# Kernel optimization log

Hardware: AMD Instinct MI355X
Metric: run time of the kernel (lower is better)

The kernel has to match this reference:

```python
import jax, jax.numpy as jnp
import numpy as np

B, S, D, H = 2, 2048, 2048, 16
DK = D // H
THETA = 10000.0


def setup_inputs() -> dict:
    key = jax.random.key(0)
    ks = jax.random.split(key, 5)
    scale = 0.02
    return {
        "x": jax.random.normal(ks[0], (B, S, D), dtype=jnp.float32),
        "W_Q": jax.random.normal(ks[1], (D, D), dtype=jnp.float32) * scale,
        "W_K": jax.random.normal(ks[2], (D, D), dtype=jnp.float32) * scale,
        "W_V": jax.random.normal(ks[3], (D, D), dtype=jnp.float32) * scale,
        "W_O": jax.random.normal(ks[4], (D, D), dtype=jnp.float32) * scale,
        "token_positions": jnp.arange(S, dtype=jnp.int32),
    }


def _rope(x, pos):
    # x: [B, S, H, DK]; pos: [S]. Interleaved-pair rotation (cs336 RoPE).
    half = DK // 2
    inv_freq = THETA ** (-(jnp.arange(half, dtype=jnp.float32) / half))  # [half]
    ang = pos.astype(jnp.float32)[:, None] * inv_freq[None, :]           # [S, half]
    cos = jnp.cos(ang)[None, :, None, :]                                 # [1,S,1,half]
    sin = jnp.sin(ang)[None, :, None, :]
    x1, x2 = x[..., ::2], x[..., 1::2]
    r1 = x1 * cos - x2 * sin
    r2 = x1 * sin + x2 * cos
    return jnp.stack([r1, r2], axis=-1).reshape(x.shape)


def reference(x, W_Q, W_K, W_V, W_O, token_positions):
    # QKV projections (Linear with no bias: y = x @ W^T)
    Q = (x @ W_Q.T).reshape(B, S, H, DK)
    K = (x @ W_K.T).reshape(B, S, H, DK)
    V = (x @ W_V.T).reshape(B, S, H, DK)
    Q = _rope(Q, token_positions)
    K = _rope(K, token_positions)
    scores = jnp.einsum("bqhd,bkhd->bhqk", Q, K) / jnp.sqrt(jnp.float32(DK))
    causal = jnp.tril(jnp.ones((S, S), dtype=bool))  # True = attend
    scores = jnp.where(causal[None, None], scores, -jnp.inf)
    attn = jax.nn.softmax(scores, axis=-1)
    out = jnp.einsum("bhqk,bkhd->bqhd", attn, V).reshape(B, S, D)
    return out @ W_O.T
```

## Files before the change

### kernel.cpp

```cpp
#include <hip/hip_runtime.h>
#include <hip/hip_bf16.h>
#include <cstdint>
#include <cstddef>

#define B_ 2
#define S_ 2048
#define D_ 2048
#define H_ 16
#define DK_ 128
#define M_ (B_*S_)

typedef __attribute__((ext_vector_type(8))) __bf16 bf16x8;
typedef __attribute__((ext_vector_type(4))) float f32x4;
typedef __attribute__((ext_vector_type(16))) float f32x16;

__device__ __forceinline__ unsigned short f2bf(float f) {
  union { float f; unsigned int u; } v; v.f = f;
  unsigned int r = (v.u + 0x7fffu + ((v.u >> 16) & 1u)) >> 16;
  return (unsigned short)r;
}
__device__ __forceinline__ float bf2f(unsigned short b) {
  union { unsigned int u; float f; } v; v.u = ((unsigned int)b) << 16;
  return v.f;
}

__device__ __forceinline__ void gld16(const void* g, void* l) {
  __builtin_amdgcn_global_load_lds(
      (const __attribute__((address_space(1))) unsigned int*)g,
      (__attribute__((address_space(3))) unsigned int*)l, 16, 0, 0);
}

__global__ void cvt_bf16(const float* __restrict__ src, unsigned short* __restrict__ dst, int n) {
  int i = (blockIdx.x * blockDim.x + threadIdx.x) * 4;
  if (i + 3 < n) {
    float4 v = *(const float4*)(src + i);
    dst[i+0] = f2bf(v.x); dst[i+1] = f2bf(v.y);
    dst[i+2] = f2bf(v.z); dst[i+3] = f2bf(v.w);
  }
}

template<int WRITE_BF16>
__global__ __launch_bounds__(512, 2) void gemm8p(const unsigned short* __restrict__ A,
                                                 const unsigned short* __restrict__ W0,
                                                 const unsigned short* __restrict__ W1,
                                                 const unsigned short* __restrict__ W2,
                                                 void* __restrict__ C0, void* __restrict__ C1,
                                                 void* __restrict__ C2,
                                                 int M, int N, int K) {
  __shared__ unsigned short sA[2][2][256 * 32];
  __shared__ unsigned short sB[2][2][256 * 32];
  const int z = blockIdx.z;
  const unsigned short* Bt = (z == 0) ? W0 : (z == 1) ? W1 : W2;
  void* Cout = (z == 0) ? C0 : (z == 1) ? C1 : C2;

  const int tid  = threadIdx.x;
  const int lane = tid & 63;
  const int wid  = tid >> 6;
  const int wm = wid >> 2, wn = wid & 3;
  const int l16 = lane & 15, quad = lane >> 4;
  const int col16 = quad ^ ((lane >> 1) & 3);
  const int qk_log = (lane & 3) ^ ((lane >> 3) & 3);
  const int srow = lane >> 2;
  const int bm = blockIdx.y * 256, bn = blockIdx.x * 256;
  const int NT = K >> 6;

  f32x4 acc[8][4];
  #pragma unroll
  for (int i = 0; i < 8; ++i)
    #pragma unroll
    for (int j = 0; j < 4; ++j)
      acc[i][j] = (f32x4){0.f, 0.f, 0.f, 0.f};

  auto stage = [&](const unsigned short* __restrict__ g, int rowbase,
                   unsigned short* l, int t, int kh) {
    const unsigned short* src = g + (size_t)rowbase * K + t * 64 + kh * 32 + qk_log * 8;
    #pragma unroll
    for (int p = 0; p < 2; ++p) {
      const int i = wid * 2 + p;
      gld16(src + (size_t)(i * 16 + srow) * K, l + i * 512);
    }
  };

  stage(A,  bm, &sA[0][0][0], 0, 0);
  stage(Bt, bn, &sB[0][0][0], 0, 0);
  stage(A,  bm, &sA[0][1][0], 0, 1);
  stage(Bt, bn, &sB[0][1][0], 0, 1);
  stage(A,  bm, &sA[1][0][0], 1, 0);
  stage(Bt, bn, &sB[1][0][0], 1, 0);
  asm volatile("s_waitcnt vmcnt(4)" ::: "memory");
  __builtin_amdgcn_s_barrier();

  for (int t = 0; t < NT; ++t) {
    const int buf = t & 1;
    bf16x8 bfrag[4];
    #pragma unroll
    for (int ph = 0; ph < 4; ++ph) {
      const int ks = ph >> 1;
      const int mh = ph & 1;
      bf16x8 afrag[4];
      const unsigned short* aP = &sA[buf][ks][0] +
          (size_t)((wm * 128 + mh * 64 + l16) * 4 + col16) * 8;
      #pragma unroll
      for (int mf = 0; mf < 4; ++mf)
        afrag[mf] = *(const bf16x8*)(aP + mf * 512);
      if (mh == 0) {
        const unsigned short* bP = &sB[buf][ks][0] +
            (size_t)((wn * 64 + l16) * 4 + col16) * 8;
        #pragma unroll
        for (int nf = 0; nf < 4; ++nf)
          bfrag[nf] = *(const bf16x8*)(bP + nf * 512);
      }
      if (ph == 0)      { if (t + 1 < NT) stage(A,  bm, &sA[buf ^ 1][1][0], t + 1, 1); }
      else if (ph == 1) { if (t + 1 < NT) stage(Bt, bn, &sB[buf ^ 1][1][0], t + 1, 1); }
      else if (ph == 2) { if (t + 2 < NT) stage(A,  bm, &sA[buf][0][0],     t + 2, 0); }
      else              { if (t + 2 < NT) stage(Bt, bn, &sB[buf][0][0],     t + 2, 0); }

      __builtin_amdgcn_s_barrier();
      asm volatile("s_waitcnt lgkmcnt(0)" ::: "memory");
      __builtin_amdgcn_s_setprio(1);
      #pragma unroll
      for (int nf = 0; nf < 4; ++nf)
        #pragma unroll
        for (int mf = 0; mf < 4; ++mf)
          acc[mh * 4 + mf][nf] = __builtin_amdgcn_mfma_f32_16x16x32_bf16(
              afrag[mf], bfrag[nf], acc[mh * 4 + mf][nf], 0, 0, 0);
      __builtin_amdgcn_s_setprio(0);
      if (ph == 3) {
        if (t + 2 < NT) asm volatile("s_waitcnt vmcnt(4)" ::: "memory");
        else            asm volatile("s_waitcnt vmcnt(0)" ::: "memory");
      }
      __builtin_amdgcn_s_barrier();
    }
  }

  #pragma unroll
  for (int mf = 0; mf < 8; ++mf) {
    const int row = bm + wm * 128 + mf * 16 + quad * 4;
    #pragma unroll
    for (int nf = 0; nf < 4; ++nf) {
      const int col = bn + wn * 64 + nf * 16 + l16;
      #pragma unroll
      for (int r = 0; r < 4; ++r) {
        if (WRITE_BF16)
          ((unsigned short*)Cout)[(size_t)(row + r) * N + col] = f2bf(acc[mf][nf][r]);
        else
          ((float*)Cout)[(size_t)(row + r) * N + col] = acc[mf][nf][r];
      }
    }
  }
}

__global__ void rope_kernel(unsigned short* __restrict__ Q, unsigned short* __restrict__ K,
                            const int* __restrict__ pos) {
  int idx = blockIdx.x * blockDim.x + threadIdx.x;
  int i = idx & 63;
  int h = (idx >> 6) & (H_ - 1);
  int s = (idx >> 10) & (S_ - 1);
  int b = idx >> 21;
  float p = (float)pos[s];
  float inv = expf(-(float)i * (9.210340371976184f / 64.0f));
  float ang = p * inv;
  float sn, cs;
  sincosf(ang, &sn, &cs);
  size_t base = (((size_t)b * S_ + s) * D_) + (size_t)h * DK_ + 2 * i;
  float x1 = bf2f(Q[base]), x2 = bf2f(Q[base + 1]);
  Q[base]     = f2bf(x1 * cs - x2 * sn);
  Q[base + 1] = f2bf(x1 * sn + x2 * cs);
  x1 = bf2f(K[base]); x2 = bf2f(K[base + 1]);
  K[base]     = f2bf(x1 * cs - x2 * sn);
  K[base + 1] = f2bf(x1 * sn + x2 * cs);
}

__global__ __launch_bounds__(256) void transpose_bf16(const unsigned short* __restrict__ src,
                                                      unsigned short* __restrict__ dst) {
  __shared__ unsigned short sT[64 * 64];
  const int b = blockIdx.y;
  const int tx = blockIdx.x & 31, ty = blockIdx.x >> 5;
  const size_t base = (size_t)b * 2048 * 2048;
  const int m0 = ty * 64, c0 = tx * 64;
  const int tid = threadIdx.x;
  #pragma unroll
  for (int c = 0; c < 2; ++c) {
    int idx = tid + c * 256;
    int row = idx >> 3;
    int chk = idx & 7;
    uint4 v = *(const uint4*)(src + base + (size_t)(m0 + row) * 2048 + c0 + chk * 8);
    *(uint4*)(sT + row * 64 + ((chk ^ (row & 7)) * 8)) = v;
  }
  __syncthreads();
  #pragma unroll
  for (int c = 0; c < 2; ++c) {
    int idx = tid + c * 256;
    int orow = idx >> 3;
    int ocol = (idx & 7) * 8;
    unsigned short tmp[8];
    #pragma unroll
    for (int j = 0; j < 8; ++j) {
      int lr = ocol + j;
      int lc = orow;
      tmp[j] = sT[lr * 64 + (((lc >> 3) ^ (lr & 7)) * 8) + (lc & 7)];
    }
    *(uint4*)(dst + base + (size_t)(c0 + orow) * 2048 + m0 + ocol) = *(const uint4*)tmp;
  }
}

__global__ __launch_bounds__(256, 2) void flash_attn(const unsigned short* __restrict__ Q,
                                                     const unsigned short* __restrict__ K,
                                                     const unsigned short* __restrict__ VT,
                                                     unsigned short* __restrict__ O) {
  __shared__ unsigned short sK[2][64 * 128];
  __shared__ unsigned short sVT[2][128 * 64];
  __shared__ unsigned short sP[4][32 * 64];

  const int tid = threadIdx.x, lane = tid & 63, wid = tid >> 6;
  const int half = lane >> 5, l32 = lane & 31;
  const int qi = 15 - (blockIdx.x & 15);
  const int bh = blockIdx.x >> 4;
  const int h = bh & (H_ - 1), b = bh >> 4;
  const int qw = qi * 128 + wid * 32;
  const size_t qkbase = ((size_t)b * S_) * D_ + (size_t)h * DK_;
  const unsigned short* Qg = Q + qkbase;
  const unsigned short* Kg = K + qkbase;
  const unsigned short* VTg = VT + (size_t)bh * DK_ * S_;
  unsigned short* Og = O + qkbase;
  unsigned short* sPw = sP[wid];

  const int kKeySub = lane >> 4;
  const int kPhys   = lane & 15;
  const int vFeatSub = lane >> 3;
  const int vPhys    = lane & 7;

  bf16x8 qf[8];
  #pragma unroll
  for (int ks = 0; ks < 8; ++ks)
    qf[ks] = *(const bf16x8*)(Qg + (size_t)(qw + l32) * D_ + ks * 16 + half * 8);

  union { unsigned short u[8]; bf16x8 v; } onesu;
  #pragma unroll
  for (int j = 0; j < 8; ++j) onesu.u[j] = 0x3F80;
  const bf16x8 ones = onesu.v;

  f32x16 Oacc[4];
  #pragma unroll
  for (int ft = 0; ft < 4; ++ft)
    #pragma unroll
    for (int r = 0; r < 16; ++r) Oacc[ft][r] = 0.f;
  f32x16 l_acc;
  #pragma unroll
  for (int r = 0; r < 16; ++r) l_acc[r] = 0.f;
  const float scale = 0.08838834764831845f;

  const int nkb = 2 * (qi + 1);

  auto stage = [&](int kb) {
    const int k0 = kb * 64;
    unsigned short* bK = sK[kb & 1];
    unsigned short* bV = sVT[kb & 1];
    #pragma unroll
    for (int p = 0; p < 4; ++p) {
      int issue = wid * 4 + p;
      int key = issue * 4 + kKeySub;
      int logiK = (kPhys & 8) | ((kPhys ^ key) & 7);
      gld16(Kg + (size_t)(k0 + key) * D_ + logiK * 8, bK + issue * 512);
      int feat = issue * 8 + vFeatSub;
      int logiV = vPhys ^ (feat & 7);
      gld16(VTg + (size_t)feat * S_ + k0 + logiV * 8, bV + issue * 512);
    }
  };

  stage(0);

  for (int kb = 0; kb < nkb; ++kb) {
    __syncthreads();
    if (kb + 1 < nkb) stage(kb + 1);

    const int k0 = kb * 64;
    if (k0 > qw + 31) continue;

    const unsigned short* bK = sK[kb & 1];
    const unsigned short* bV = sVT[kb & 1];

    f32x16 sc[2];
    #pragma unroll
    for (int t = 0; t < 2; ++t)
      #pragma unroll
      for (int r = 0; r < 16; ++r) sc[t][r] = 0.f;
    #pragma unroll
    for (int ks = 0; ks < 8; ++ks) {
      const int logi = ks * 2 + half;
      #pragma unroll
      for (int t = 0; t < 2; ++t) {
        const int key = t * 32 + l32;
        const int phys = (logi & 8) | ((logi ^ key) & 7);
        bf16x8 kf = *(const bf16x8*)(bK + key * 128 + phys * 8);
        sc[t] = __builtin_amdgcn_mfma_f32_32x32x16_bf16(qf[ks], kf, sc[t], 0, 0, 0);
      }
    }

    const bool diag = (k0 + 63 > qw);
    #pragma unroll
    for (int t = 0; t < 2; ++t) {
      const int col = t * 32 + l32;
      const int keyg = k0 + col;
      #pragma unroll
      for (int r = 0; r < 16; ++r) {
        const int rl = (r & 3) + 8 * (r >> 2) + 4 * half;
        float v = sc[t][r] * scale;
        if (diag && (keyg > qw + rl)) v = -1e30f;
        sPw[rl * 64 + (((col >> 3) ^ (rl & 7)) * 8) + (col & 7)] = f2bf(__expf(v));
      }
    }

    #pragma unroll
    for (int ksp = 0; ksp < 4; ++ksp) {
      const int logi = ksp * 2 + half;
      bf16x8 pf = *(const bf16x8*)(sPw + l32 * 64 + ((logi ^ (l32 & 7)) * 8));
      l_acc = __builtin_amdgcn_mfma_f32_32x32x16_bf16(pf, ones, l_acc, 0, 0, 0);
      #pragma unroll
      for (int ft = 0; ft < 4; ++ft) {
        const int feat = ft * 32 + l32;
        const int phys = logi ^ (feat & 7);
        bf16x8 vf = *(const bf16x8*)(bV + feat * 64 + phys * 8);
        Oacc[ft] = __builtin_amdgcn_mfma_f32_32x32x16_bf16(pf, vf, Oacc[ft], 0, 0, 0);
      }
    }
  }

  #pragma unroll
  for (int ft = 0; ft < 4; ++ft) {
    const int feat = ft * 32 + l32;
    #pragma unroll
    for (int r = 0; r < 16; ++r) {
      const int rl = (r & 3) + 8 * (r >> 2) + 4 * half;
      Og[(size_t)(qw + rl) * D_ + feat] = f2bf(Oacc[ft][r] / l_acc[r]);
    }
  }
}

extern "C" void kernel_launch(void* const* d_in, const int* in_sizes, int n_in,
                              void* d_out, int out_size, void* d_ws, size_t ws_size,
                              hipStream_t stream) {
  const float* x  = (const float*)d_in[0];
  const float* Wq = (const float*)d_in[1];
  const float* Wk = (const float*)d_in[2];
  const float* Wv = (const float*)d_in[3];
  const float* Wo = (const float*)d_in[4];
  const int*  pos = (const int*)d_in[5];
  float* out = (float*)d_out;

  char* ws = (char*)d_ws;
  size_t off = 0;
  auto alloc = [&](size_t bytes) { void* p = ws + off; off += (bytes + 255) & ~255ULL; return p; };
  const size_t nx = (size_t)M_ * D_;
  const size_t nw = (size_t)D_ * D_;
  unsigned short* xb  = (unsigned short*)alloc(nx * 2);
  unsigned short* wqb = (unsigned short*)alloc(nw * 2);
  unsigned short* wkb = (unsigned short*)alloc(nw * 2);
  unsigned short* wvb = (unsigned short*)alloc(nw * 2);
  unsigned short* wob = (unsigned short*)alloc(nw * 2);
  unsigned short* Qb  = (unsigned short*)alloc(nx * 2);
  unsigned short* Kb  = (unsigned short*)alloc(nx * 2);
  unsigned short* Vb  = (unsigned short*)alloc(nx * 2);
  unsigned short* AOb = xb;
  unsigned short* VTb = wqb;

  hipLaunchKernelGGL(cvt_bf16, dim3(nx / 1024), dim3(256), 0, stream, x,  xb,  (int)nx);
  hipLaunchKernelGGL(cvt_bf16, dim3(nw / 1024), dim3(256), 0, stream, Wq, wqb, (int)nw);
  hipLaunchKernelGGL(cvt_bf16, dim3(nw / 1024), dim3(256), 0, stream, Wk, wkb, (int)nw);
  hipLaunchKernelGGL(cvt_bf16, dim3(nw / 1024), dim3(256), 0, stream, Wv, wvb, (int)nw);
  hipLaunchKernelGGL(cvt_bf16, dim3(nw / 1024), dim3(256), 0, stream, Wo, wob, (int)nw);

  hipLaunchKernelGGL((gemm8p<1>), dim3(D_ / 256, M_ / 256, 3), dim3(512), 0, stream,
                     xb, wqb, wkb, wvb, (void*)Qb, (void*)Kb, (void*)Vb, M_, D_, D_);

  hipLaunchKernelGGL(rope_kernel, dim3((B_ * S_ * H_ * 64) / 256), dim3(256), 0, stream, Qb, Kb, pos);

  hipLaunchKernelGGL(transpose_bf16, dim3(1024, 2), dim3(256), 0, stream, Vb, VTb);

  hipLaunchKernelGGL(flash_attn, dim3(B_ * H_ * (S_ / 128)), dim3(256), 0, stream, Qb, Kb, VTb, AOb);

  hipLaunchKernelGGL((gemm8p<0>), dim3(D_ / 256, M_ / 256, 1), dim3(512), 0, stream,
                     AOb, wob, wob, wob, (void*)out, (void*)out, (void*)out, M_, D_, D_);
}
```

Baseline: 455.8 us.

## Use 128x128 tile GEMM for output projection and rebalance attention block order

The output projection switches from the 256x256-tile gemm8p kernel to a new, simpler 128x128-tile gemm_bt kernel, which launches 512 blocks instead of 128 so that more compute units are filled. The flash attention grid now uses descending query-block order for the first half of the blocks and ascending order for the second half, to spread causal work more evenly. The new GEMM has no software pipelining or double buffering and syncs twice per 32-wide K step, so its per-block efficiency may be lower.

```diff
diff --git a/kernel.cpp b/kernel.cpp
--- a/kernel.cpp
+++ b/kernel.cpp
@@ -145,6 +145,77 @@
           ((unsigned short*)Cout)[(size_t)(row + r) * N + col] = f2bf(acc[mf][nf][r]);
         else
           ((float*)Cout)[(size_t)(row + r) * N + col] = acc[mf][nf][r];
+      }
+    }
+  }
+}
+
+template<int WRITE_BF16>
+__global__ __launch_bounds__(256) void gemm_bt(const unsigned short* __restrict__ A,
+                                               const unsigned short* __restrict__ W0,
+                                               const unsigned short* __restrict__ W1,
+                                               const unsigned short* __restrict__ W2,
+                                               void* __restrict__ C0, void* __restrict__ C1,
+                                               void* __restrict__ C2,
+                                               int M, int N, int K) {
+  __shared__ unsigned short sA[128 * 32];
+  __shared__ unsigned short sB[128 * 32];
+  const int z = blockIdx.z;
+  const unsigned short* Bt = (z == 0) ? W0 : (z == 1) ? W1 : W2;
+  void* Cout = (z == 0) ? C0 : (z == 1) ? C1 : C2;
+
+  const int tid  = threadIdx.x;
+  const int lane = tid & 63;
+  const int wid  = tid >> 6;
+  const int wm = wid >> 1, wn = wid & 1;
+  const int quad = lane >> 4, l16 = lane & 15;
+  const int bm = blockIdx.y * 128, bn = blockIdx.x * 128;
+  const int srow = lane >> 2;
+  const int scol = (lane & 3) * 8;
+
+  f32x4 acc[4][4];
+  #pragma unroll
+  for (int i = 0; i < 4; ++i)
+    #pragma unroll
+    for (int j = 0; j < 4; ++j)
+      acc[i][j] = (f32x4){0.f, 0.f, 0.f, 0.f};
+
+  for (int k0 = 0; k0 < K; k0 += 32) {
+    __syncthreads();
+    #pragma unroll
+    for (int p = 0; p < 2; ++p) {
+      int row = p * 64 + wid * 16;
+      gld16(A  + (size_t)(bm + row + srow) * K + k0 + scol, sA + row * 32);
+      gld16(Bt + (size_t)(bn + row + srow) * K + k0 + scol, sB + row * 32);
+    }
+    __syncthreads();
+
+    bf16x8 af[4], bfr[4];
+    #pragma unroll
+    for (int i = 0; i < 4; ++i)
+      af[i] = *(const bf16x8*)(sA + (wm * 64 + i * 16 + l16) * 32 + quad * 8);
+    #pragma unroll
+    for (int j = 0; j < 4; ++j)
+      bfr[j] = *(const bf16x8*)(sB + (wn * 64 + j * 16 + l16) * 32 + quad * 8);
+    #pragma unroll
+    for (int i = 0; i < 4; ++i)
+      #pragma unroll
+      for (int j = 0; j < 4; ++j)
+        acc[i][j] = __builtin_amdgcn_mfma_f32_16x16x32_bf16(af[i], bfr[j], acc[i][j], 0, 0, 0);
+  }
+
+  #pragma unroll
+  for (int i = 0; i < 4; ++i) {
+    int row = bm + wm * 64 + i * 16 + quad * 4;
+    #pragma unroll
+    for (int j = 0; j < 4; ++j) {
+      int col = bn + wn * 64 + j * 16 + l16;
+      #pragma unroll
+      for (int r = 0; r < 4; ++r) {
+        if (WRITE_BF16)
+          ((unsigned short*)Cout)[(size_t)(row + r) * N + col] = f2bf(acc[i][j][r]);
+        else
+          ((float*)Cout)[(size_t)(row + r) * N + col] = acc[i][j][r];
       }
     }
   }
@@ -214,8 +285,10 @@
 
   const int tid = threadIdx.x, lane = tid & 63, wid = tid >> 6;
   const int half = lane >> 5, l32 = lane & 31;
-  const int qi = 15 - (blockIdx.x & 15);
-  const int bh = blockIdx.x >> 4;
+  const int x = blockIdx.x;
+  const int j = x & 15;
+  const int bh = x >> 4;
+  const int qi = (x < 256) ? (15 - j) : j;
   const int h = bh & (H_ - 1), b = bh >> 4;
   const int qw = qi * 128 + wid * 32;
   const size_t qkbase = ((size_t)b * S_) * D_ + (size_t)h * DK_;
@@ -237,7 +310,7 @@
 
   union { unsigned short u[8]; bf16x8 v; } onesu;
   #pragma unroll
-  for (int j = 0; j < 8; ++j) onesu.u[j] = 0x3F80;
+  for (int j2 = 0; j2 < 8; ++j2) onesu.u[j2] = 0x3F80;
   const bf16x8 ones = onesu.v;
 
   f32x16 Oacc[4];
@@ -379,6 +452,6 @@
 
   hipLaunchKernelGGL(flash_attn, dim3(B_ * H_ * (S_ / 128)), dim3(256), 0, stream, Qb, Kb, VTb, AOb);
 
-  hipLaunchKernelGGL((gemm8p<0>), dim3(D_ / 256, M_ / 256, 1), dim3(512), 0, stream,
+  hipLaunchKernelGGL((gemm_bt<0>), dim3(D_ / 128, M_ / 128, 1), dim3(256), 0, stream,
                      AOb, wob, wob, wob, (void*)out, (void*)out, (void*)out, M_, D_, D_);
 }
```

After: 447.7 us. No clear change (-1.8%).
